# Kernel optimization log

Measured on AMD Instinct MI355X. Metric: run time of the kernel, lower is better.

Reference implementation:

```python
import jax, jax.numpy as jnp
import numpy as np

MAX_DET = 300   # max_det in non_max_suppression
IMG = 640       # input image H=W
MH = MW = 160   # proto mask resolution
NM = 32         # mask coefficients
ALPHA = 0.6
MARGIN = 15


def setup_inputs() -> dict:
    key = jax.random.key(0)
    k1, k2, k3, k4, k5, k6 = jax.random.split(key, 6)
    na = 8400
    # realistic YOLOv8 raw head output: xywh in pixels, 1 class score in (0,1), 32 mask coeffs
    cxcy = jax.random.uniform(k1, (1, 2, na), minval=0.0, maxval=float(IMG))
    wh = jax.random.uniform(k2, (1, 2, na), minval=10.0, maxval=200.0)
    cls = jax.random.uniform(k3, (1, 1, na))
    mcoef = jax.random.normal(k4, (1, NM, na))
    prediction = jnp.concatenate([cxcy, wh, cls, mcoef], axis=1)  # [1,37,8400]
    proto = jax.random.normal(k5, (1, NM, MH, MW))
    img = jax.random.uniform(k6, (1, 3, IMG, IMG))
    return {"prediction": prediction, "proto": proto, "img": img,
            "conf_thres": jnp.float32(0.25), "iou_thres": jnp.float32(0.45)}


def _xywh2xyxy(x):
    cx, cy, w, h = x[..., 0], x[..., 1], x[..., 2], x[..., 3]
    return jnp.stack([cx - w / 2, cy - h / 2, cx + w / 2, cy + h / 2], axis=-1)


def _box_iou(b):  # b: [K,4] xyxy -> [K,K] pairwise IoU (torchvision convention)
    x1, y1, x2, y2 = b[:, 0], b[:, 1], b[:, 2], b[:, 3]
    area = (x2 - x1) * (y2 - y1)
    iw = jnp.clip(jnp.minimum(x2[:, None], x2[None, :]) - jnp.maximum(x1[:, None], x1[None, :]), 0)
    ih = jnp.clip(jnp.minimum(y2[:, None], y2[None, :]) - jnp.maximum(y1[:, None], y1[None, :]), 0)
    inter = iw * ih
    return inter / (area[:, None] + area[None, :] - inter + 1e-7)


def _nms_keep(iou, valid, iou_thres):
    # sequential greedy suppression over score-sorted boxes (padded, fixed K)
    K = iou.shape[0]
    def body(keep, i):
        suppressed = jnp.any(keep & (iou[i] > iou_thres))
        keep = keep.at[i].set(valid[i] & ~suppressed)
        return keep, None
    keep, _ = jax.lax.scan(body, jnp.zeros((K,), bool), jnp.arange(K))
    return keep


def reference(prediction, proto, img, conf_thres, iou_thres):
    # --- decode: [1,37,na] -> [na,37], xywh->xyxy (bs=1, nc=1, class offset c = 0*max_wh = 0)
    p = prediction[0].T                      # [na,37]
    boxes = _xywh2xyxy(p[:, :4])             # [na,4]
    conf = p[:, 4]                           # nc=1 -> max over classes is the class itself, j=0
    mcoef = p[:, 5:]                         # [na,32]
    valid = conf > conf_thres
    score = jnp.where(valid, conf, -1.0)
    order = jnp.argsort(-score)[:MAX_DET]    # top max_det candidates by confidence
    boxes_k, score_k, m_k = boxes[order], score[order], mcoef[order]
    valid_k = valid[order]
    # --- NMS (padded)
    keep = _nms_keep(_box_iou(boxes_k), valid_k, iou_thres)  # [K] bool
    # --- process_mask: linear combine protos, sigmoid, crop, bilinear upsample, >0.5
    masks = jax.nn.sigmoid(m_k @ proto[0].reshape(NM, -1)).reshape(MAX_DET, MH, MW)
    scale = jnp.array([MW / IMG, MH / IMG, MW / IMG, MH / IMG], dtype=boxes_k.dtype)
    db = boxes_k * scale                     # downsampled bboxes [K,4]
    r = jnp.arange(MW, dtype=masks.dtype)[None, None, :]
    c = jnp.arange(MH, dtype=masks.dtype)[None, :, None]
    crop = ((r >= db[:, 0, None, None]) & (r < db[:, 2, None, None]) &
            (c >= db[:, 1, None, None]) & (c < db[:, 3, None, None]))
    masks = masks * crop
    masks_up = jax.image.resize(masks, (MAX_DET, IMG, IMG), method='linear')  # align_corners=False bilinear
    masks_bin = (masks_up > 0.5) & keep[:, None, None]       # invalid/suppressed rows zeroed
    # --- scale_boxes: img1_shape == img0_shape -> gain=1, pad=0, just clip
    boxes_c = jnp.clip(boxes_k, 0.0, float(IMG))
    results = jnp.concatenate([boxes_c, score_k[:, None], jnp.zeros((MAX_DET, 1), boxes_c.dtype)], axis=1)
    results = results * keep[:, None].astype(results.dtype)  # [K,6] padded detections
    # --- max-area box -> crop window coords
    areas = jnp.where(keep, (boxes_c[:, 2] - boxes_c[:, 0]) * (boxes_c[:, 3] - boxes_c[:, 1]), 0.0)
    mb = jnp.where(jnp.any(keep), boxes_c[jnp.argmax(areas)], jnp.zeros(4, boxes_c.dtype))
    y1 = jnp.maximum(mb[1].astype(jnp.int32) - MARGIN, 0)
    y2 = jnp.minimum(mb[3].astype(jnp.int32) + MARGIN, IMG)
    x1 = jnp.maximum(mb[0].astype(jnp.int32) - MARGIN, 0)
    x2 = jnp.minimum(mb[2].astype(jnp.int32) + MARGIN, IMG)
    crop_coords = jnp.stack([y1, y2, x1, x2])
    # --- mask overlay blending (stack over images, sum over detections)
    stacked_mk = jnp.sum(masks_bin.astype(img.dtype), axis=0)[None]  # [1,640,640]
    pixels = jnp.count_nonzero(stacked_mk)
    blue = jnp.zeros((3, IMG, IMG), img.dtype).at[2].set(1.0)
    img_out = (1.0 - stacked_mk) * img + stacked_mk * (ALPHA * img + (1.0 - ALPHA) * blue)
    return results, keep, masks_bin, pixels, img_out, crop_coords
```

## Files before the change

### kernel.cpp

```cpp
#include <hip/hip_runtime.h>
#include <stdint.h>

#define NA 8400
#define MAXD 300
#define NMC 32
#define IMGD 640
#define MH 160
#define MW 160
#define PROTO_HW (MH*MW)
#define IMG_HW (IMGD*IMGD)

#define OFF_RESULTS 0
#define OFF_KEEP    1800
#define OFF_MASKS   2100
#define OFF_PIXELS  (2100 + 300*IMG_HW)
#define OFF_IMG     (OFF_PIXELS + 1)
#define OFF_CROP    (OFF_IMG + 3*IMG_HW)

#define WSO_MASKS160 0
#define WSO_KEYS     (MAXD*PROTO_HW*4)
#define WSO_HIST     (WSO_KEYS + NA*8)
#define WSO_META     (WSO_HIST + 1024*4)
#define WSO_ORDER    (WSO_META + 64)
#define WSO_VFLAG    (WSO_ORDER + MAXD*4)
#define WSO_SCORE    (WSO_VFLAG + MAXD*4)
#define WSO_BOXES    (WSO_SCORE + MAXD*4)
#define WSO_MCOEF    (WSO_BOXES + MAXD*16)
#define WSO_KEEPI    (WSO_MCOEF + MAXD*NMC*4)
#define WSO_KLIST    (WSO_KEEPI + MAXD*4)
#define WSO_EBOX     (WSO_KLIST + MAXD*4)

__global__ __launch_bounds__(256)
void k_score(const float* __restrict__ pred, const float* __restrict__ conf_thres_p,
             uint64_t* __restrict__ keys, unsigned* __restrict__ hist) {
    int i = blockIdx.x * 256 + threadIdx.x;
    if (i >= NA) return;
    float th = *conf_thres_p;
    float conf = pred[4 * NA + i];
    uint64_t key = 0;
    if (conf > th) {
        unsigned fb = __float_as_uint(conf);
        key = ((uint64_t)fb << 32) | (unsigned)(NA - 1 - i);
        int bin = (int)(conf * 1024.0f);
        bin = bin < 0 ? 0 : (bin > 1023 ? 1023 : bin);
        atomicAdd(&hist[bin], 1u);
    }
    keys[i] = key;
}

__global__ __launch_bounds__(1024)
void k_select(const float* __restrict__ pred, const uint64_t* __restrict__ keys,
              const unsigned* __restrict__ hist,
              int* __restrict__ order, int* __restrict__ vflag, float* __restrict__ score_k,
              float* __restrict__ boxes_k, float* __restrict__ mcoef_k) {
    __shared__ unsigned cum[1024];
    __shared__ uint64_t kl[2048];
    __shared__ int s_cnt, s_bcut, s_nsel;
    __shared__ int sorder[MAXD];
    __shared__ int svf[MAXD];
    int t = threadIdx.x;

    cum[t] = hist[t];
    __syncthreads();
    for (int off = 1; off < 1024; off <<= 1) {
        unsigned v = cum[t] + ((t + off < 1024) ? cum[t + off] : 0u);
        __syncthreads();
        cum[t] = v;
        __syncthreads();
    }
    if (t == 0) {
        s_cnt = 0;
        int tot = (int)cum[0];
        s_nsel = tot < MAXD ? tot : MAXD;
        s_bcut = 0;
    }
    __syncthreads();
    int nsel = s_nsel;
    if (nsel > 0) {
        if (cum[t] >= (unsigned)nsel && (t == 1023 || cum[t + 1] < (unsigned)nsel))
            s_bcut = t;
    }
    __syncthreads();
    int bcut = s_bcut;
    if (nsel > 0) {
        for (int i = t; i < NA; i += 1024) {
            uint64_t key = keys[i];
            if (key) {
                float conf = __uint_as_float((unsigned)(key >> 32));
                int bin = (int)(conf * 1024.0f);
                bin = bin > 1023 ? 1023 : bin;
                if (bin >= bcut) {
                    int p = atomicAdd(&s_cnt, 1);
                    if (p < 2048) kl[p] = key;
                }
            }
        }
    }
    __syncthreads();
    int cnt = s_cnt < 2048 ? s_cnt : 2048;
    for (int i = t; i < 2048; i += 1024)
        if (i >= cnt) kl[i] = 0;
    __syncthreads();
    for (int k = 2; k <= 2048; k <<= 1) {
        for (int j = k >> 1; j > 0; j >>= 1) {
            int i = ((t & ~(j - 1)) << 1) | (t & (j - 1));
            int p = i | j;
            bool desc = ((i & k) == 0);
            uint64_t a = kl[i], b = kl[p];
            if ((a < b) == desc) { kl[i] = b; kl[p] = a; }
            __syncthreads();
        }
    }
    if (t < MAXD) {
        int v = (t < nsel) ? 1 : 0;
        uint64_t key = v ? kl[t] : 0;
        int idx = v ? (NA - 1 - (int)(key & 0xffffffffu)) : 0;
        sorder[t] = idx; svf[t] = v;
        order[t] = idx; vflag[t] = v;
        score_k[t] = v ? __uint_as_float((unsigned)(key >> 32)) : -1.0f;
        float cx = pred[0 * NA + idx], cy = pred[1 * NA + idx];
        float w = pred[2 * NA + idx], h = pred[3 * NA + idx];
        float b0 = cx - w * 0.5f, b1 = cy - h * 0.5f, b2 = cx + w * 0.5f, b3 = cy + h * 0.5f;
        if (!v) { b0 = b1 = b2 = b3 = 0.f; }
        boxes_k[t * 4 + 0] = b0; boxes_k[t * 4 + 1] = b1;
        boxes_k[t * 4 + 2] = b2; boxes_k[t * 4 + 3] = b3;
    }
    __syncthreads();
    for (int m = t; m < MAXD * NMC; m += 1024) {
        int r = m >> 5, c = m & 31;
        mcoef_k[m] = svf[r] ? pred[(5 + c) * NA + sorder[r]] : 0.f;
    }
}

__global__ __launch_bounds__(512)
void k_nms(const float* __restrict__ iou_thres_p, const int* __restrict__ vflag,
           const float* __restrict__ boxes_k, const float* __restrict__ score_k,
           int* __restrict__ keepi, int* __restrict__ klist, int* __restrict__ meta,
           int* __restrict__ ebox, float* __restrict__ out) {
    __shared__ uint64_t su[MAXD][5];
    __shared__ float bx[MAXD][4];
    __shared__ float sarea[MAXD];
    __shared__ int sv[MAXD];
    __shared__ int skeep[MAXD];
    int t = threadIdx.x;
    for (int i = t; i < MAXD; i += 512) {
        float b0 = boxes_k[i * 4 + 0], b1 = boxes_k[i * 4 + 1];
        float b2 = boxes_k[i * 4 + 2], b3 = boxes_k[i * 4 + 3];
        bx[i][0] = b0; bx[i][1] = b1; bx[i][2] = b2; bx[i][3] = b3;
        sarea[i] = (b2 - b0) * (b3 - b1);
        sv[i] = vflag[i];
    }
    __syncthreads();
    float ithr = *iou_thres_p;
    if (t < MAXD) {
        float x1 = bx[t][0], y1 = bx[t][1], x2 = bx[t][2], y2 = bx[t][3];
        float ar = sarea[t];
        uint64_t m[5] = {0, 0, 0, 0, 0};
        for (int j = 0; j < MAXD; j++) {
            float iw = fmaxf(fminf(x2, bx[j][2]) - fmaxf(x1, bx[j][0]), 0.f);
            float ih = fmaxf(fminf(y2, bx[j][3]) - fmaxf(y1, bx[j][1]), 0.f);
            float inter = iw * ih;
            float iou = inter / (ar + sarea[j] - inter + 1e-7f);
            if (iou > ithr) m[j >> 6] |= 1ull << (j & 63);
        }
        for (int w = 0; w < 5; w++) su[t][w] = m[w];

        float db0 = x1 * 0.25f, db1 = y1 * 0.25f, db2 = x2 * 0.25f, db3 = y2 * 0.25f;
        int pxmin = max(0, (int)ceilf(db0));
        int pxmax = min(MW - 1, (int)ceilf(db2) - 1);
        int pymin = max(0, (int)ceilf(db1));
        int pymax = min(MH - 1, (int)ceilf(db3) - 1);
        int xlo = 1, xhi = 0, ylo = 1, yhi = 0;
        if (pxmin <= pxmax && pymin <= pymax) {
            xlo = max(0, 4 * pxmin - 2); xhi = min(IMGD - 1, 4 * pxmax + 5);
            ylo = max(0, 4 * pymin - 2); yhi = min(IMGD - 1, 4 * pymax + 5);
        }
        ebox[t * 4 + 0] = xlo; ebox[t * 4 + 1] = xhi;
        ebox[t * 4 + 2] = ylo; ebox[t * 4 + 3] = yhi;
    }
    __syncthreads();
    if (t < 64) {
        uint64_t kwl = 0;
        int lane = t;
        for (int i = 0; i < MAXD; i++) {
            uint64_t x = (lane < 5) ? (su[i][lane] & kwl) : 0;
            bool sup = __any(x != 0);
            bool k = sv[i] && !sup;
            if (lane == (i >> 6) && k) kwl |= 1ull << (i & 63);
            if (lane == 0) { skeep[i] = k ? 1 : 0; keepi[i] = k ? 1 : 0; }
        }
    }
    __syncthreads();
    if (t < MAXD) {
        bool k = skeep[t] != 0;
        float bc0 = fminf(fmaxf(bx[t][0], 0.f), 640.f);
        float bc1 = fminf(fmaxf(bx[t][1], 0.f), 640.f);
        float bc2 = fminf(fmaxf(bx[t][2], 0.f), 640.f);
        float bc3 = fminf(fmaxf(bx[t][3], 0.f), 640.f);
        out[OFF_RESULTS + t * 6 + 0] = k ? bc0 : 0.f;
        out[OFF_RESULTS + t * 6 + 1] = k ? bc1 : 0.f;
        out[OFF_RESULTS + t * 6 + 2] = k ? bc2 : 0.f;
        out[OFF_RESULTS + t * 6 + 3] = k ? bc3 : 0.f;
        out[OFF_RESULTS + t * 6 + 4] = k ? score_k[t] : 0.f;
        out[OFF_RESULTS + t * 6 + 5] = 0.f;
        out[OFF_KEEP + t] = k ? 1.f : 0.f;
    }
    if (t == 0) {
        int n = 0;
        bool anyk = false;
        for (int i = 0; i < MAXD; i++)
            if (skeep[i]) { klist[n++] = i; anyk = true; }
        meta[0] = n;
        float amax = -INFINITY; int ai = 0;
        for (int i = 0; i < MAXD; i++) {
            float bc0 = fminf(fmaxf(bx[i][0], 0.f), 640.f);
            float bc1 = fminf(fmaxf(bx[i][1], 0.f), 640.f);
            float bc2 = fminf(fmaxf(bx[i][2], 0.f), 640.f);
            float bc3 = fminf(fmaxf(bx[i][3], 0.f), 640.f);
            float a = skeep[i] ? (bc2 - bc0) * (bc3 - bc1) : 0.f;
            if (a > amax) { amax = a; ai = i; }
        }
        float mb0 = 0.f, mb1 = 0.f, mb2 = 0.f, mb3 = 0.f;
        if (anyk) {
            mb0 = fminf(fmaxf(bx[ai][0], 0.f), 640.f);
            mb1 = fminf(fmaxf(bx[ai][1], 0.f), 640.f);
            mb2 = fminf(fmaxf(bx[ai][2], 0.f), 640.f);
            mb3 = fminf(fmaxf(bx[ai][3], 0.f), 640.f);
        }
        int y1 = max((int)mb1 - 15, 0);
        int y2 = min((int)mb3 + 15, IMGD);
        int x1 = max((int)mb0 - 15, 0);
        int x2 = min((int)mb2 + 15, IMGD);
        out[OFF_CROP + 0] = (float)y1;
        out[OFF_CROP + 1] = (float)y2;
        out[OFF_CROP + 2] = (float)x1;
        out[OFF_CROP + 3] = (float)x2;
    }
}

__global__ __launch_bounds__(256)
void k_masks(const float* __restrict__ proto, const float* __restrict__ mcoef_k,
             const float* __restrict__ boxes_k, const int* __restrict__ keepi,
             float* __restrict__ masks160) {
    int slot = blockIdx.y;
    if (!keepi[slot]) return;
    __shared__ float co[NMC];
    __shared__ float db[4];
    int t = threadIdx.x;
    if (t < NMC) co[t] = mcoef_k[slot * NMC + t];
    if (t >= NMC && t < NMC + 4) db[t - NMC] = boxes_k[slot * 4 + (t - NMC)] * 0.25f;
    __syncthreads();
    int p = blockIdx.x * 256 + t;
    float acc = 0.f;
#pragma unroll
    for (int k = 0; k < NMC; k++) acc = fmaf(co[k], proto[k * PROTO_HW + p], acc);
    float sig = 1.f / (1.f + expf(-acc));
    int py = p / MW, px = p - py * MW;
    float r = (float)px, c = (float)py;
    bool crop = (r >= db[0]) && (r < db[2]) && (c >= db[1]) && (c < db[3]);
    masks160[slot * PROTO_HW + p] = crop ? sig : 0.f;
}

__device__ __forceinline__ float bilin(const float* __restrict__ m, int y, int x) {
    float sy = 0.25f * (float)y - 0.375f;
    float sx = 0.25f * (float)x - 0.375f;
    int y0 = (int)floorf(sy); float fy = sy - (float)y0;
    int x0 = (int)floorf(sx); float fx = sx - (float)x0;
    if (y0 < 0) { y0 = 0; fy = 0.f; }
    int y1 = y0 + 1; if (y1 > MH - 1) { y1 = MH - 1; fy = 0.f; }
    if (x0 < 0) { x0 = 0; fx = 0.f; }
    int x1 = x0 + 1; if (x1 > MW - 1) { x1 = MW - 1; fx = 0.f; }
    const float* r0 = m + y0 * MW;
    const float* r1 = m + y1 * MW;
    float v00 = r0[x0], v01 = r0[x1], v10 = r1[x0], v11 = r1[x1];
    float t0 = fmaf(fy, v10, (1.f - fy) * v00);
    float t1 = fmaf(fy, v11, (1.f - fy) * v01);
    return fmaf(fx, t1, (1.f - fx) * t0);
}

__global__ __launch_bounds__(256)
void k_upsample(const float* __restrict__ masks160, const int* __restrict__ keepi,
                const int* __restrict__ ebox, float* __restrict__ out_masks) {
    int det = blockIdx.y;
    int base = (blockIdx.x * 256 + threadIdx.x) * 4;
    float4 o = {0.f, 0.f, 0.f, 0.f};
    if (keepi[det]) {
        int y = base / IMGD;
        int x = base - y * IMGD;
        int xlo = ebox[det * 4 + 0], xhi = ebox[det * 4 + 1];
        int ylo = ebox[det * 4 + 2], yhi = ebox[det * 4 + 3];
        if (y >= ylo && y <= yhi && x + 3 >= xlo && x <= xhi) {
            const float* m = masks160 + (size_t)det * PROTO_HW;
            o.x = (bilin(m, y, x)     > 0.5f) ? 1.f : 0.f;
            o.y = (bilin(m, y, x + 1) > 0.5f) ? 1.f : 0.f;
            o.z = (bilin(m, y, x + 2) > 0.5f) ? 1.f : 0.f;
            o.w = (bilin(m, y, x + 3) > 0.5f) ? 1.f : 0.f;
        }
    }
    *(float4*)(out_masks + (size_t)det * IMG_HW + base) = o;
}

__global__ __launch_bounds__(256)
void k_blend(const float* __restrict__ masks160, const int* __restrict__ klist,
             const int* __restrict__ ebox, const int* __restrict__ meta,
             const float* __restrict__ img, float* __restrict__ out,
             int* __restrict__ pix_count) {
    __shared__ int sxlo[MAXD], sxhi[MAXD], sylo[MAXD], syhi[MAXD], soff[MAXD];
    int n = meta[0];
    int t = threadIdx.x;
    for (int i = t; i < n; i += 256) {
        int d = klist[i];
        sxlo[i] = ebox[d * 4 + 0]; sxhi[i] = ebox[d * 4 + 1];
        sylo[i] = ebox[d * 4 + 2]; syhi[i] = ebox[d * 4 + 3];
        soff[i] = d * PROTO_HW;
    }
    __syncthreads();
    int base = (blockIdx.x * 256 + t) * 4;
    int y = base / IMGD, x = base - y * IMGD;
    float4 s = {0.f, 0.f, 0.f, 0.f};
    for (int i = 0; i < n; i++) {
        if (y >= sylo[i] && y <= syhi[i] && x + 3 >= sxlo[i] && x <= sxhi[i]) {
            const float* m = masks160 + soff[i];
            s.x += (bilin(m, y, x)     > 0.5f) ? 1.f : 0.f;
            s.y += (bilin(m, y, x + 1) > 0.5f) ? 1.f : 0.f;
            s.z += (bilin(m, y, x + 2) > 0.5f) ? 1.f : 0.f;
            s.w += (bilin(m, y, x + 3) > 0.5f) ? 1.f : 0.f;
        }
    }
#pragma unroll
    for (int c = 0; c < 3; c++) {
        float4 iv = *(const float4*)(img + c * IMG_HW + base);
        float bl = (c == 2) ? 1.f : 0.f;
        float4 ov;
        ov.x = (1.f - s.x) * iv.x + s.x * (0.6f * iv.x + 0.4f * bl);
        ov.y = (1.f - s.y) * iv.y + s.y * (0.6f * iv.y + 0.4f * bl);
        ov.z = (1.f - s.z) * iv.z + s.z * (0.6f * iv.z + 0.4f * bl);
        ov.w = (1.f - s.w) * iv.w + s.w * (0.6f * iv.w + 0.4f * bl);
        *(float4*)(out + OFF_IMG + c * IMG_HW + base) = ov;
    }
    int cnt = (s.x != 0.f) + (s.y != 0.f) + (s.z != 0.f) + (s.w != 0.f);
    for (int o2 = 32; o2 > 0; o2 >>= 1) cnt += __shfl_down(cnt, o2, 64);
    if ((t & 63) == 0) atomicAdd(pix_count, cnt);
}

__global__ void k_final(const int* __restrict__ meta, float* __restrict__ out) {
    out[OFF_PIXELS] = (float)meta[1];
}

extern "C" void kernel_launch(void* const* d_in, const int* in_sizes, int n_in,
                              void* d_out, int out_size, void* d_ws, size_t ws_size,
                              hipStream_t stream) {
    const float* pred       = (const float*)d_in[0];
    const float* proto      = (const float*)d_in[1];
    const float* img        = (const float*)d_in[2];
    const float* conf_thres = (const float*)d_in[3];
    const float* iou_thres  = (const float*)d_in[4];
    float* out = (float*)d_out;
    char* ws = (char*)d_ws;

    float*    masks160 = (float*)(ws + WSO_MASKS160);
    uint64_t* keys     = (uint64_t*)(ws + WSO_KEYS);
    unsigned* hist     = (unsigned*)(ws + WSO_HIST);
    int*      meta     = (int*)(ws + WSO_META);
    int*      order    = (int*)(ws + WSO_ORDER);
    int*      vflag    = (int*)(ws + WSO_VFLAG);
    float*    score_k  = (float*)(ws + WSO_SCORE);
    float*    boxes_k  = (float*)(ws + WSO_BOXES);
    float*    mcoef_k  = (float*)(ws + WSO_MCOEF);
    int*      keepi    = (int*)(ws + WSO_KEEPI);
    int*      klist    = (int*)(ws + WSO_KLIST);
    int*      ebox     = (int*)(ws + WSO_EBOX);

    hipMemsetAsync(ws + WSO_HIST, 0, 1024 * 4 + 64, stream);

    k_score<<<dim3((NA + 255) / 256), dim3(256), 0, stream>>>(pred, conf_thres, keys, hist);
    k_select<<<dim3(1), dim3(1024), 0, stream>>>(pred, keys, hist, order, vflag, score_k, boxes_k, mcoef_k);
    k_nms<<<dim3(1), dim3(512), 0, stream>>>(iou_thres, vflag, boxes_k, score_k, keepi, klist, meta, ebox, out);
    k_masks<<<dim3(PROTO_HW / 256, MAXD), dim3(256), 0, stream>>>(proto, mcoef_k, boxes_k, keepi, masks160);
    k_upsample<<<dim3(IMG_HW / 1024, MAXD), dim3(256), 0, stream>>>(masks160, keepi, ebox, out + OFF_MASKS);
    k_blend<<<dim3(IMG_HW / 1024), dim3(256), 0, stream>>>(masks160, klist, ebox, meta, img, out, meta + 1);
    k_final<<<dim3(1), dim3(1), 0, stream>>>(meta, out);
}
```

Before: 760.7 us.

## Fuse mask zero-fill into score kernel, paint only box regions, rank-sort selection

The score kernel now also zero-fills the full 300x640x640 output mask tensor using extra blocks, so the previously per-pixel upsample kernel only has to paint pixels inside each kept detection's expanded box. Dead detections return immediately. The bitonic sort over 2048 keys is replaced by an O(n^2) rank-count that scatters the top 300. This removes most of the bilinear and branch work and the full-grid launch over dead detections, but the zero-fill still writes the whole buffer. The rank sort may cost more when many candidates pass the cut.

```diff
diff --git a/kernel.cpp b/kernel.cpp
--- a/kernel.cpp
+++ b/kernel.cpp
@@ -30,10 +30,22 @@
 #define WSO_KLIST    (WSO_KEEPI + MAXD*4)
 #define WSO_EBOX     (WSO_KLIST + MAXD*4)
 
+#define NSB 33
+#define NFILL 30000
+
 __global__ __launch_bounds__(256)
-void k_score(const float* __restrict__ pred, const float* __restrict__ conf_thres_p,
-             uint64_t* __restrict__ keys, unsigned* __restrict__ hist) {
-    int i = blockIdx.x * 256 + threadIdx.x;
+void k_score_fill(const float* __restrict__ pred, const float* __restrict__ conf_thres_p,
+                  uint64_t* __restrict__ keys, unsigned* __restrict__ hist,
+                  float* __restrict__ out_masks) {
+    int bid = blockIdx.x;
+    if (bid >= NSB) {
+        size_t f = (size_t)(bid - NSB) * 4096 + (size_t)threadIdx.x * 16;
+        float4 z = {0.f, 0.f, 0.f, 0.f};
+        float4* p = (float4*)(out_masks + f);
+        p[0] = z; p[1] = z; p[2] = z; p[3] = z;
+        return;
+    }
+    int i = bid * 256 + threadIdx.x;
     if (i >= NA) return;
     float th = *conf_thres_p;
     float conf = pred[4 * NA + i];
@@ -51,10 +63,11 @@
 __global__ __launch_bounds__(1024)
 void k_select(const float* __restrict__ pred, const uint64_t* __restrict__ keys,
               const unsigned* __restrict__ hist,
-              int* __restrict__ order, int* __restrict__ vflag, float* __restrict__ score_k,
+              int* __restrict__ vflag, float* __restrict__ score_k,
               float* __restrict__ boxes_k, float* __restrict__ mcoef_k) {
     __shared__ unsigned cum[1024];
     __shared__ uint64_t kl[2048];
+    __shared__ uint64_t srt[MAXD];
     __shared__ int s_cnt, s_bcut, s_nsel;
     __shared__ int sorder[MAXD];
     __shared__ int svf[MAXD];
@@ -98,25 +111,19 @@
     }
     __syncthreads();
     int cnt = s_cnt < 2048 ? s_cnt : 2048;
-    for (int i = t; i < 2048; i += 1024)
-        if (i >= cnt) kl[i] = 0;
-    __syncthreads();
-    for (int k = 2; k <= 2048; k <<= 1) {
-        for (int j = k >> 1; j > 0; j >>= 1) {
-            int i = ((t & ~(j - 1)) << 1) | (t & (j - 1));
-            int p = i | j;
-            bool desc = ((i & k) == 0);
-            uint64_t a = kl[i], b = kl[p];
-            if ((a < b) == desc) { kl[i] = b; kl[p] = a; }
-            __syncthreads();
-        }
-    }
+    for (int c = t; c < cnt; c += 1024) {
+        uint64_t key = kl[c];
+        int rank = 0;
+        for (int j = 0; j < cnt; j++) rank += (kl[j] > key) ? 1 : 0;
+        if (rank < MAXD) srt[rank] = key;
+    }
+    __syncthreads();
     if (t < MAXD) {
         int v = (t < nsel) ? 1 : 0;
-        uint64_t key = v ? kl[t] : 0;
+        uint64_t key = v ? srt[t] : 0;
         int idx = v ? (NA - 1 - (int)(key & 0xffffffffu)) : 0;
         sorder[t] = idx; svf[t] = v;
-        order[t] = idx; vflag[t] = v;
+        vflag[t] = v;
         score_k[t] = v ? __uint_as_float((unsigned)(key >> 32)) : -1.0f;
         float cx = pred[0 * NA + idx], cy = pred[1 * NA + idx];
         float w = pred[2 * NA + idx], h = pred[3 * NA + idx];
@@ -279,25 +286,28 @@
 }
 
 __global__ __launch_bounds__(256)
-void k_upsample(const float* __restrict__ masks160, const int* __restrict__ keepi,
-                const int* __restrict__ ebox, float* __restrict__ out_masks) {
+void k_paint(const float* __restrict__ masks160, const int* __restrict__ keepi,
+             const int* __restrict__ ebox, float* __restrict__ out_masks) {
     int det = blockIdx.y;
-    int base = (blockIdx.x * 256 + threadIdx.x) * 4;
-    float4 o = {0.f, 0.f, 0.f, 0.f};
-    if (keepi[det]) {
-        int y = base / IMGD;
-        int x = base - y * IMGD;
-        int xlo = ebox[det * 4 + 0], xhi = ebox[det * 4 + 1];
-        int ylo = ebox[det * 4 + 2], yhi = ebox[det * 4 + 3];
-        if (y >= ylo && y <= yhi && x + 3 >= xlo && x <= xhi) {
-            const float* m = masks160 + (size_t)det * PROTO_HW;
+    if (!keepi[det]) return;
+    int xlo = ebox[det * 4 + 0], xhi = ebox[det * 4 + 1];
+    int ylo = ebox[det * 4 + 2], yhi = ebox[det * 4 + 3];
+    if (xlo > xhi || ylo > yhi) return;
+    int xlo0 = xlo & ~3;
+    int q = blockIdx.x * 256 + threadIdx.x;
+    int rx = q % 56, ry = q / 56;
+    const float* m = masks160 + (size_t)det * PROTO_HW;
+    float* od = out_masks + (size_t)det * IMG_HW;
+    for (int y = ylo + ry; y <= yhi; y += 224) {
+        for (int x = xlo0 + 4 * rx; x <= xhi; x += 224) {
+            float4 o;
             o.x = (bilin(m, y, x)     > 0.5f) ? 1.f : 0.f;
             o.y = (bilin(m, y, x + 1) > 0.5f) ? 1.f : 0.f;
             o.z = (bilin(m, y, x + 2) > 0.5f) ? 1.f : 0.f;
             o.w = (bilin(m, y, x + 3) > 0.5f) ? 1.f : 0.f;
-        }
-    }
-    *(float4*)(out_masks + (size_t)det * IMG_HW + base) = o;
+            *(float4*)(od + y * IMGD + x) = o;
+        }
+    }
 }
 
 __global__ __launch_bounds__(256)
@@ -362,7 +372,6 @@
     uint64_t* keys     = (uint64_t*)(ws + WSO_KEYS);
     unsigned* hist     = (unsigned*)(ws + WSO_HIST);
     int*      meta     = (int*)(ws + WSO_META);
-    int*      order    = (int*)(ws + WSO_ORDER);
     int*      vflag    = (int*)(ws + WSO_VFLAG);
     float*    score_k  = (float*)(ws + WSO_SCORE);
     float*    boxes_k  = (float*)(ws + WSO_BOXES);
@@ -373,11 +382,12 @@
 
     hipMemsetAsync(ws + WSO_HIST, 0, 1024 * 4 + 64, stream);
 
-    k_score<<<dim3((NA + 255) / 256), dim3(256), 0, stream>>>(pred, conf_thres, keys, hist);
-    k_select<<<dim3(1), dim3(1024), 0, stream>>>(pred, keys, hist, order, vflag, score_k, boxes_k, mcoef_k);
+    k_score_fill<<<dim3(NSB + NFILL), dim3(256), 0, stream>>>(pred, conf_thres, keys, hist,
+                                                              out + OFF_MASKS);
+    k_select<<<dim3(1), dim3(1024), 0, stream>>>(pred, keys, hist, vflag, score_k, boxes_k, mcoef_k);
     k_nms<<<dim3(1), dim3(512), 0, stream>>>(iou_thres, vflag, boxes_k, score_k, keepi, klist, meta, ebox, out);
     k_masks<<<dim3(PROTO_HW / 256, MAXD), dim3(256), 0, stream>>>(proto, mcoef_k, boxes_k, keepi, masks160);
-    k_upsample<<<dim3(IMG_HW / 1024, MAXD), dim3(256), 0, stream>>>(masks160, keepi, ebox, out + OFF_MASKS);
+    k_paint<<<dim3(49, MAXD), dim3(256), 0, stream>>>(masks160, keepi, ebox, out + OFF_MASKS);
     k_blend<<<dim3(IMG_HW / 1024), dim3(256), 0, stream>>>(masks160, klist, ebox, meta, img, out, meta + 1);
     k_final<<<dim3(1), dim3(1), 0, stream>>>(meta, out);
 }
```

New measurement: 811.9 us. 1.07x slower.
